# Kernel tuning notes

Hardware: AMD Instinct MI355X
Metric: run time of the kernel (lower is better)

Reference implementation:

```python
import jax, jax.numpy as jnp
import numpy as np

B, S, D, H, F = 2, 2048, 1024, 16, 4096
DH = D // H
EPS = 1e-6


def setup_inputs() -> dict:
    key = jax.random.key(0)
    ks = jax.random.split(key, 8)
    x = jax.random.normal(ks[0], (B, S, D), dtype=jnp.float32)
    # causal mask, broadcastable over [B,H,S,S]
    attention_mask = jnp.tril(jnp.ones((S, S), dtype=bool))[None, None]
    Wqkv = jax.random.normal(ks[1], (3 * D, D), dtype=jnp.float32) * (1.0 / np.sqrt(D))
    Wout = jax.random.normal(ks[2], (D, D), dtype=jnp.float32) * (1.0 / np.sqrt(D))
    W1 = jax.random.normal(ks[3], (F, D), dtype=jnp.float32) * (1.0 / np.sqrt(D))
    b1 = jnp.zeros((F,), dtype=jnp.float32)
    W2 = jax.random.normal(ks[4], (D, F), dtype=jnp.float32) * (1.0 / np.sqrt(F))
    b2 = jnp.zeros((D,), dtype=jnp.float32)
    gamma1 = jnp.ones((D,), dtype=jnp.float32)
    beta1 = jnp.zeros((D,), dtype=jnp.float32)
    gamma2 = jnp.ones((D,), dtype=jnp.float32)
    beta2 = jnp.zeros((D,), dtype=jnp.float32)
    return {"x": x, "attention_mask": attention_mask, "Wqkv": Wqkv, "Wout": Wout,
            "W1": W1, "b1": b1, "W2": W2, "b2": b2,
            "gamma1": gamma1, "beta1": beta1, "gamma2": gamma2, "beta2": beta2}


def layer_norm(x, gamma, beta):
    # Matches torch module: (x - mean) / (std + eps), std unbiased=False
    mean = jnp.mean(x, axis=-1, keepdims=True)
    std = jnp.sqrt(jnp.mean((x - mean) ** 2, axis=-1, keepdims=True))
    return gamma * ((x - mean) / (std + EPS)) + beta


def reference(x, attention_mask, Wqkv, Wout, W1, b1, W2, b2, gamma1, beta1, gamma2, beta2):
    # --- attention sub-block (Pre-LN) ---
    h = layer_norm(x, gamma1, beta1)
    qkv = h @ Wqkv.T                                   # [B,S,3D]
    qkv = qkv.reshape(B, S, 3, H, DH).transpose(2, 0, 3, 1, 4)  # [3,B,H,S,DH]
    q, k, v = qkv[0], qkv[1], qkv[2]
    scale = DH ** -0.5
    scores = jnp.einsum('bhqd,bhkd->bhqk', q, k) * scale
    scores = jnp.where(attention_mask, scores, -jnp.inf)
    attn = jax.nn.softmax(scores, axis=-1)
    out = jnp.einsum('bhqk,bhkd->bhqd', attn, v)       # [B,H,S,DH]
    out = out.transpose(0, 2, 1, 3).reshape(B, S, D)
    out = out @ Wout.T
    x = x + out                                        # dropout eval = identity
    # --- FFN sub-block (Pre-LN) ---
    h = layer_norm(x, gamma2, beta2)
    h = jax.nn.gelu(h @ W1.T + b1, approximate=False)  # torch GELU default = exact erf
    h = h @ W2.T + b2
    return x + h
```

## Files before the change

### kernel.cpp

```cpp
#include <hip/hip_runtime.h>
#include <hip/hip_bf16.h>
#include <math.h>


typedef __bf16 bf16;
typedef __bf16 bf16x4 __attribute__((ext_vector_type(4)));
typedef __bf16 bf16x8 __attribute__((ext_vector_type(8)));
typedef float f32x4 __attribute__((ext_vector_type(4)));

#define LOG2E 1.4426950408889634f
#define NSHIFT -17.312340489f

__device__ __forceinline__ f32x4 mfma16(bf16x8 a, bf16x8 b, f32x4 c) {
    return __builtin_amdgcn_mfma_f32_16x16x32_bf16(a, b, c, 0, 0, 0);
}
__device__ __forceinline__ void load16_lds(const bf16* g, bf16* l) {
    __builtin_amdgcn_global_load_lds(
        (__attribute__((address_space(1))) void*)g,
        (__attribute__((address_space(3))) void*)l, 16, 0, 0);
}

__global__ __launch_bounds__(256) void cvt4_kernel(const float* __restrict__ s0,
                                                   const float* __restrict__ s1,
                                                   const float* __restrict__ s2,
                                                   const float* __restrict__ s3,
                                                   bf16* __restrict__ dst) {
    const int blk = blockIdx.x;
    const float* s;
    int base;
    if (blk < 3072)      { s = s0; base = blk * 1024; }
    else if (blk < 4096) { s = s1; base = (blk - 3072) * 1024; }
    else if (blk < 8192) { s = s2; base = (blk - 4096) * 1024; }
    else                 { s = s3; base = (blk - 8192) * 1024; }
    const int t4 = threadIdx.x * 4;
    const float4 f = *(const float4*)(s + base + t4);
    bf16x4 o;
    o[0] = (bf16)f.x; o[1] = (bf16)f.y; o[2] = (bf16)f.z; o[3] = (bf16)f.w;
    *(bf16x4*)(dst + (size_t)blk * 1024 + t4) = o;
}

__global__ __launch_bounds__(256) void ln_kernel(const float* __restrict__ xin,
                                                 bf16* __restrict__ out,
                                                 const float* __restrict__ gamma,
                                                 const float* __restrict__ beta) {
    const int row = blockIdx.x;
    const int tid = threadIdx.x;
    const float4 f = *(const float4*)(xin + (size_t)row * 1024 + tid * 4);
    float v[4] = {f.x, f.y, f.z, f.w};
    float s = v[0] + v[1] + v[2] + v[3];
    float s2 = v[0] * v[0] + v[1] * v[1] + v[2] * v[2] + v[3] * v[3];
#pragma unroll
    for (int off = 1; off < 64; off <<= 1) {
        s += __shfl_xor(s, off);
        s2 += __shfl_xor(s2, off);
    }
    __shared__ float red[8];
    const int wave = tid >> 6, lane = tid & 63;
    if (lane == 0) { red[wave] = s; red[4 + wave] = s2; }
    __syncthreads();
    s = red[0] + red[1] + red[2] + red[3];
    s2 = red[4] + red[5] + red[6] + red[7];
    const float mean = s * (1.0f / 1024.0f);
    float var = s2 * (1.0f / 1024.0f) - mean * mean;
    var = fmaxf(var, 0.0f);
    const float rstd = 1.0f / (sqrtf(var) + 1e-6f);
    const int c = tid * 4;
    const float4 g = *(const float4*)(gamma + c);
    const float4 b = *(const float4*)(beta + c);
    bf16x4 o;
    o[0] = (bf16)((v[0] - mean) * rstd * g.x + b.x);
    o[1] = (bf16)((v[1] - mean) * rstd * g.y + b.y);
    o[2] = (bf16)((v[2] - mean) * rstd * g.z + b.z);
    o[3] = (bf16)((v[3] - mean) * rstd * g.w + b.w);
    *(bf16x4*)(out + (size_t)row * 1024 + c) = o;
}

#define STAGE(tt, bi)                                              \
    do {                                                           \
        const int _k0 = (tt) << 5;                                 \
        load16_lds(Ap + _k0, &As[bi][tid * 8]);                    \
        load16_lds(Bp + _k0, &Bs[bi][tid * 8]);                    \
        load16_lds(Ap + rstep + _k0, &As[bi][tid * 8 + 2048]);     \
        load16_lds(Bp + rstep + _k0, &Bs[bi][tid * 8 + 2048]);     \
    } while (0)

template <int EPI>
__global__ __launch_bounds__(256, 3) void gemm_bt(const bf16* __restrict__ A,
                                                  const bf16* __restrict__ B,
                                                  int N, int K, int ldk,
                                                  bf16* __restrict__ outb,
                                                  float* __restrict__ outf,
                                                  const float* __restrict__ bias,
                                                  const float* __restrict__ resf,
                                                  bf16* __restrict__ qk,
                                                  bf16* __restrict__ vt) {
    __shared__ alignas(16) bf16 As[3][128 * 32];
    __shared__ alignas(16) bf16 Bs[3][128 * 32];
    const int tid = threadIdx.x;
    const int bm = blockIdx.x, bn = blockIdx.y;
    const int wave = tid >> 6, lane = tid & 63;
    const int wm = (wave >> 1) * 64, wn = (wave & 1) * 64;
    const int l16 = lane & 15, quad = lane >> 4;

    f32x4 acc[4][4] = {};

    const size_t koff = (size_t)blockIdx.z * K;
    const int row0 = tid >> 2, ch0 = tid & 3;
    const int gch = ch0 ^ ((row0 >> 1) & 3);
    const bf16* Ap = A + (size_t)(bm * 128 + row0) * ldk + koff + gch * 8;
    const bf16* Bp = B + (size_t)(bn * 128 + row0) * ldk + koff + gch * 8;
    const size_t rstep = (size_t)64 * ldk;

    const int nt = K >> 5;

    STAGE(0, 0);
    STAGE(1, 1);
    asm volatile("s_waitcnt vmcnt(4)" ::: "memory");
    __builtin_amdgcn_s_barrier();
    asm volatile("" ::: "memory");

    int i0 = 0, i1 = 1, i2 = 2;
    for (int t = 0; t < nt; ++t) {
        if (t + 2 < nt) STAGE(t + 2, i2);

        bf16x8 af[4], bfr[4];
#pragma unroll
        for (int i = 0; i < 4; i++) {
            const int ra = wm + i * 16 + l16;
            af[i] = *(const bf16x8*)(&As[i0][ra * 32 + (quad ^ ((ra >> 1) & 3)) * 8]);
        }
#pragma unroll
        for (int j = 0; j < 4; j++) {
            const int rb = wn + j * 16 + l16;
            bfr[j] = *(const bf16x8*)(&Bs[i0][rb * 32 + (quad ^ ((rb >> 1) & 3)) * 8]);
        }
        __builtin_amdgcn_s_setprio(1);
#pragma unroll
        for (int i = 0; i < 4; i++)
#pragma unroll
            for (int j = 0; j < 4; j++) acc[i][j] = mfma16(af[i], bfr[j], acc[i][j]);
        __builtin_amdgcn_s_setprio(0);

        if (t + 2 < nt) {
            asm volatile("s_waitcnt vmcnt(4)" ::: "memory");
        } else if (t + 1 < nt) {
            asm volatile("s_waitcnt vmcnt(0)" ::: "memory");
        }
        if (t + 1 < nt) {
            __builtin_amdgcn_s_barrier();
            asm volatile("" ::: "memory");
        }
        const int tmp = i0; i0 = i1; i1 = i2; i2 = tmp;
    }

#pragma unroll
    for (int i = 0; i < 4; i++) {
#pragma unroll
        for (int j = 0; j < 4; j++) {
            const int gr0 = bm * 128 + wm + i * 16 + quad * 4;
            const int gc = bn * 128 + wn + j * 16 + l16;
            float bv = 0.0f;
            if (EPI == 2) bv = bias[gc];
            if (EPI == 5 && bias && blockIdx.z == 0) bv = bias[gc];
            if (EPI == 4 && gc >= 2048) {
                const int n = gc - 2048;
                const int hh = n >> 6, dd = n & 63;
                const int bb = gr0 >> 11, ss = gr0 & 2047;
                bf16x4 pk;
#pragma unroll
                for (int r = 0; r < 4; r++) pk[r] = (bf16)acc[i][j][r];
                *(bf16x4*)(vt + ((size_t)((bb * 16 + hh) * 64 + dd)) * 2048 + ss) = pk;
            } else {
#pragma unroll
                for (int r = 0; r < 4; r++) {
                    const float v = acc[i][j][r];
                    const size_t idx = (size_t)(gr0 + r) * N + gc;
                    if (EPI == 0) {
                        outb[idx] = (bf16)v;
                    } else if (EPI == 1) {
                        outf[idx] = v + resf[idx];
                    } else if (EPI == 2) {
                        const float t = v + bv;
                        outb[idx] = (bf16)(0.5f * t * (1.0f + erff(t * 0.70710678118654752f)));
                    } else if (EPI == 5) {
                        atomicAdd(&outf[idx], v + bv);
                    } else {
                        qk[(size_t)(gr0 + r) * 2048 + gc] = (bf16)v;
                    }
                }
            }
        }
    }
}
#undef STAGE

__global__ __launch_bounds__(256, 4) void flash_attn(const bf16* __restrict__ qk,
                                                     const bf16* __restrict__ vt,
                                                     bf16* __restrict__ attn) {
    __shared__ alignas(16) bf16 Ks[64 * 72];
    __shared__ alignas(16) bf16 Vs[64 * 72];
    __shared__ alignas(16) bf16 Ps[4][16 * 72];
    const int tid = threadIdx.x;
    const int wave = tid >> 6, lane = tid & 63;
    const int l16 = lane & 15, quad = lane >> 4;
    const int bh = blockIdx.x;
    const int qt = 31 - blockIdx.y;
    const int b = bh >> 4, h = bh & 15;
    const int q0w = qt * 64 + wave * 16;
    const bf16* qkb = qk + (size_t)b * 2048 * 2048;
    const bf16* vtb = vt + (size_t)bh * 64 * 2048;

    bf16x8 qf[2];
#pragma unroll
    for (int c = 0; c < 2; c++) {
        bf16x8 v = *(const bf16x8*)(qkb + (size_t)(q0w + l16) * 2048 +
                                    h * 64 + c * 32 + quad * 8);
#pragma unroll
        for (int e = 0; e < 8; e++) v[e] = (bf16)((float)v[e] * 0.125f);
        qf[c] = v;
    }

    float lsum[4] = {0.0f, 0.0f, 0.0f, 0.0f};
    f32x4 o[4] = {};

    const int ntiles = qt + 1;
    for (int t = 0; t < ntiles; t++) {
        const int k0 = t * 64;
#pragma unroll
        for (int i = 0; i < 2; i++) {
            const int r = i * 32 + (tid >> 3), ch = tid & 7;
            *(uint4*)(&Ks[r * 72 + ch * 8]) =
                *(const uint4*)(qkb + (size_t)(k0 + r) * 2048 + 1024 + h * 64 + ch * 8);
            *(uint4*)(&Vs[r * 72 + ch * 8]) =
                *(const uint4*)(vtb + (size_t)r * 2048 + k0 + ch * 8);
        }
        __syncthreads();
        f32x4 s[4];
#pragma unroll
        for (int kt = 0; kt < 4; kt++) {
            const bf16x8 k0f = *(const bf16x8*)(&Ks[(kt * 16 + l16) * 72 + quad * 8]);
            const bf16x8 k1f = *(const bf16x8*)(&Ks[(kt * 16 + l16) * 72 + 32 + quad * 8]);
            s[kt] = mfma16(qf[1], k1f, mfma16(qf[0], k0f, (f32x4){0, 0, 0, 0}));
        }
        const bool need_mask = (t == ntiles - 1);
#pragma unroll
        for (int r = 0; r < 4; r++) {
            const int qrow = q0w + quad * 4 + r;
            float e0 = exp2f(fmaf(s[0][r], LOG2E, NSHIFT));
            float e1 = exp2f(fmaf(s[1][r], LOG2E, NSHIFT));
            float e2 = exp2f(fmaf(s[2][r], LOG2E, NSHIFT));
            float e3 = exp2f(fmaf(s[3][r], LOG2E, NSHIFT));
            if (need_mask) {
                if (k0 + l16 > qrow) e0 = 0.0f;
                if (k0 + 16 + l16 > qrow) e1 = 0.0f;
                if (k0 + 32 + l16 > qrow) e2 = 0.0f;
                if (k0 + 48 + l16 > qrow) e3 = 0.0f;
            }
            lsum[r] += (e0 + e1) + (e2 + e3);
            bf16* pp = &Ps[wave][(quad * 4 + r) * 72];
            pp[l16] = (bf16)e0;
            pp[16 + l16] = (bf16)e1;
            pp[32 + l16] = (bf16)e2;
            pp[48 + l16] = (bf16)e3;
        }
#pragma unroll
        for (int c = 0; c < 2; c++) {
            const bf16x8 pf = *(const bf16x8*)(&Ps[wave][l16 * 72 + c * 32 + quad * 8]);
#pragma unroll
            for (int dt = 0; dt < 4; dt++) {
                const bf16x8 vf =
                    *(const bf16x8*)(&Vs[(dt * 16 + l16) * 72 + c * 32 + quad * 8]);
                o[dt] = mfma16(pf, vf, o[dt]);
            }
        }
        __syncthreads();
    }

#pragma unroll
    for (int r = 0; r < 4; r++) {
#pragma unroll
        for (int off = 1; off < 16; off <<= 1) lsum[r] += __shfl_xor(lsum[r], off);
        lsum[r] = 1.0f / fmaxf(lsum[r], 1e-30f);
    }
    bf16* ob = attn + (size_t)b * 2048 * 1024;
#pragma unroll
    for (int dt = 0; dt < 4; dt++)
#pragma unroll
        for (int r = 0; r < 4; r++) {
            const int q = q0w + quad * 4 + r;
            ob[(size_t)q * 1024 + h * 64 + dt * 16 + l16] = (bf16)(o[dt][r] * lsum[r]);
        }
}

extern "C" void kernel_launch(void* const* d_in, const int* in_sizes, int n_in,
                              void* d_out, int out_size, void* d_ws, size_t ws_size,
                              hipStream_t stream) {
    const float* x    = (const float*)d_in[0];
    const float* Wqkv = (const float*)d_in[2];
    const float* Wout = (const float*)d_in[3];
    const float* W1   = (const float*)d_in[4];
    const float* b1   = (const float*)d_in[5];
    const float* W2   = (const float*)d_in[6];
    const float* b2   = (const float*)d_in[7];
    const float* g1   = (const float*)d_in[8];
    const float* be1  = (const float*)d_in[9];
    const float* g2   = (const float*)d_in[10];
    const float* be2  = (const float*)d_in[11];

    char* ws = (char*)d_ws;
    bf16* Wb     = (bf16*)(ws);
    bf16* Wqkv_b = (bf16*)(ws);
    bf16* Wout_b = (bf16*)(ws + (6u << 20));
    bf16* W1_b   = (bf16*)(ws + (8u << 20));
    bf16* W2_b   = (bf16*)(ws + (16u << 20));
    bf16* h      = (bf16*)(ws + (24u << 20));
    bf16* qkbuf  = (bf16*)(ws + (32u << 20));
    bf16* vtbuf  = (bf16*)(ws + (48u << 20));
    bf16* attn   = (bf16*)(ws + (56u << 20));
    bf16* act    = (bf16*)(ws + (32u << 20));
    float* x2    = (float*)d_out;

    cvt4_kernel<<<12288, 256, 0, stream>>>(Wqkv, Wout, W1, W2, Wb);

    ln_kernel<<<4096, 256, 0, stream>>>(x, h, g1, be1);
    gemm_bt<4><<<dim3(32, 24), 256, 0, stream>>>(h, Wqkv_b, 3072, 1024, 1024,
                                                 nullptr, nullptr, nullptr, nullptr,
                                                 qkbuf, vtbuf);
    flash_attn<<<dim3(32, 32), 256, 0, stream>>>(qkbuf, vtbuf, attn);
    gemm_bt<1><<<dim3(32, 8), 256, 0, stream>>>(attn, Wout_b, 1024, 1024, 1024,
                                                nullptr, x2, nullptr, x, nullptr, nullptr);
    ln_kernel<<<4096, 256, 0, stream>>>(x2, h, g2, be2);
    gemm_bt<2><<<dim3(32, 32), 256, 0, stream>>>(h, W1_b, 4096, 1024, 1024,
                                                 act, nullptr, b1, nullptr, nullptr, nullptr);
    gemm_bt<5><<<dim3(32, 8, 2), 256, 0, stream>>>(act, W2_b, 1024, 2048, 4096,
                                                   nullptr, x2, b2, nullptr, nullptr, nullptr);
}
```

Baseline: 392.6 us.

## Add 256x256 eight-wave multi-phase GEMM for QKV and FFN projections

Adds a new GEMM kernel with 256x256 block tiles, 512 threads (8 waves), BK=64 split into two 32-wide halves, double-buffered LDS, and global-to-LDS loads interleaved between four barrier-delimited MFMA phases. It is used for the QKV, FFN1 and FFN2 GEMMs. The W2 GEMM moves from split-K 2 to split-K 4 with atomic accumulation, and the old kernel is kept only for the residual output projection. Larger tiles improve operand reuse and the phased schedule overlaps memory traffic with MFMA. In exchange, grids get much smaller (e.g. 192 or 256 blocks), which can leave CUs idle, and there are more barriers and more atomics.

```diff
diff --git a/kernel.cpp b/kernel.cpp
--- a/kernel.cpp
+++ b/kernel.cpp
@@ -84,16 +84,11 @@
         load16_lds(Bp + rstep + _k0, &Bs[bi][tid * 8 + 2048]);     \
     } while (0)
 
-template <int EPI>
-__global__ __launch_bounds__(256, 3) void gemm_bt(const bf16* __restrict__ A,
-                                                  const bf16* __restrict__ B,
-                                                  int N, int K, int ldk,
-                                                  bf16* __restrict__ outb,
-                                                  float* __restrict__ outf,
-                                                  const float* __restrict__ bias,
-                                                  const float* __restrict__ resf,
-                                                  bf16* __restrict__ qk,
-                                                  bf16* __restrict__ vt) {
+__global__ __launch_bounds__(256, 3) void gemm_res(const bf16* __restrict__ A,
+                                                   const bf16* __restrict__ B,
+                                                   int N, int K, int ldk,
+                                                   float* __restrict__ outf,
+                                                   const float* __restrict__ resf) {
     __shared__ alignas(16) bf16 As[3][128 * 32];
     __shared__ alignas(16) bf16 Bs[3][128 * 32];
     const int tid = threadIdx.x;
@@ -104,11 +99,10 @@
 
     f32x4 acc[4][4] = {};
 
-    const size_t koff = (size_t)blockIdx.z * K;
     const int row0 = tid >> 2, ch0 = tid & 3;
     const int gch = ch0 ^ ((row0 >> 1) & 3);
-    const bf16* Ap = A + (size_t)(bm * 128 + row0) * ldk + koff + gch * 8;
-    const bf16* Bp = B + (size_t)(bn * 128 + row0) * ldk + koff + gch * 8;
+    const bf16* Ap = A + (size_t)(bm * 128 + row0) * ldk + gch * 8;
+    const bf16* Bp = B + (size_t)(bn * 128 + row0) * ldk + gch * 8;
     const size_t rstep = (size_t)64 * ldk;
 
     const int nt = K >> 5;
@@ -154,11 +148,163 @@
     }
 
 #pragma unroll
-    for (int i = 0; i < 4; i++) {
+    for (int i = 0; i < 4; i++)
 #pragma unroll
         for (int j = 0; j < 4; j++) {
             const int gr0 = bm * 128 + wm + i * 16 + quad * 4;
             const int gc = bn * 128 + wn + j * 16 + l16;
+#pragma unroll
+            for (int r = 0; r < 4; r++) {
+                const size_t idx = (size_t)(gr0 + r) * N + gc;
+                outf[idx] = acc[i][j][r] + resf[idx];
+            }
+        }
+}
+#undef STAGE
+
+#define STG_A(bb, rk, tt)                                          \
+    do {                                                           \
+        const int _ko = ((tt) << 6) + ((rk) << 5);                 \
+        load16_lds(Ap + _ko, &As[bb][rk][tid * 8]);                \
+        load16_lds(Ap + rstep + _ko, &As[bb][rk][4096 + tid * 8]); \
+    } while (0)
+#define STG_B(bb, rk, tt)                                          \
+    do {                                                           \
+        const int _ko = ((tt) << 6) + ((rk) << 5);                 \
+        load16_lds(Bp + _ko, &Bs[bb][rk][tid * 8]);                \
+        load16_lds(Bp + rstep + _ko, &Bs[bb][rk][4096 + tid * 8]); \
+    } while (0)
+#define PHASE_OPEN()                       \
+    __builtin_amdgcn_s_barrier();          \
+    asm volatile("" ::: "memory");         \
+    __builtin_amdgcn_s_setprio(1)
+#define PHASE_CLOSE()                      \
+    __builtin_amdgcn_s_setprio(0);         \
+    __builtin_amdgcn_s_barrier();          \
+    asm volatile("" ::: "memory")
+
+template <int EPI>
+__global__ __launch_bounds__(512, 2) void gemm256_8ph(const bf16* __restrict__ A,
+                                                      const bf16* __restrict__ B,
+                                                      int N, int K, int ldk,
+                                                      bf16* __restrict__ outb,
+                                                      float* __restrict__ outf,
+                                                      const float* __restrict__ bias,
+                                                      bf16* __restrict__ qk,
+                                                      bf16* __restrict__ vt) {
+    __shared__ alignas(16) bf16 As[2][2][8192];
+    __shared__ alignas(16) bf16 Bs[2][2][8192];
+    const int tid = threadIdx.x;
+    const int bm = blockIdx.x, bn = blockIdx.y;
+    const int wave = tid >> 6, lane = tid & 63;
+    const int wm = (wave >> 2) * 128, wn = (wave & 3) * 64;
+    const int l16 = lane & 15, quad = lane >> 4;
+
+    f32x4 acc[8][4] = {};
+
+    const size_t koff = (size_t)blockIdx.z * K;
+    const int row0 = tid >> 2;
+    const int gch = (tid & 3) ^ (row0 & 3);
+    const bf16* Ap = A + (size_t)(bm * 256 + row0) * ldk + koff + gch * 8;
+    const bf16* Bp = B + (size_t)(bn * 256 + row0) * ldk + koff + gch * 8;
+    const size_t rstep = (size_t)128 * ldk;
+
+    const int NT = K >> 6;
+
+    STG_A(0, 0, 0); STG_B(0, 0, 0); STG_A(0, 1, 0); STG_B(0, 1, 0);
+    STG_A(1, 0, 1); STG_B(1, 0, 1); STG_A(1, 1, 1);
+    asm volatile("s_waitcnt vmcnt(6)" ::: "memory");
+    __builtin_amdgcn_s_barrier();
+    asm volatile("" ::: "memory");
+
+    for (int t = 0; t < NT; ++t) {
+        const int buf = t & 1;
+        bf16x8 af[8], bj0, bj1;
+
+#pragma unroll
+        for (int i = 0; i < 8; i++) {
+            const int ra = wm + i * 16 + l16;
+            af[i] = *(const bf16x8*)&As[buf][0][ra * 32 + (quad ^ (ra & 3)) * 8];
+        }
+        {
+            const int rb0 = wn + l16, rb1 = wn + 16 + l16;
+            bj0 = *(const bf16x8*)&Bs[buf][0][rb0 * 32 + (quad ^ (rb0 & 3)) * 8];
+            bj1 = *(const bf16x8*)&Bs[buf][0][rb1 * 32 + (quad ^ (rb1 & 3)) * 8];
+        }
+        if (t + 1 < NT) STG_B(buf ^ 1, 1, t + 1);
+        PHASE_OPEN();
+#pragma unroll
+        for (int i = 0; i < 8; i++) {
+            acc[i][0] = mfma16(af[i], bj0, acc[i][0]);
+            acc[i][1] = mfma16(af[i], bj1, acc[i][1]);
+        }
+        PHASE_CLOSE();
+
+        {
+            const int rb2 = wn + 32 + l16, rb3 = wn + 48 + l16;
+            bj0 = *(const bf16x8*)&Bs[buf][0][rb2 * 32 + (quad ^ (rb2 & 3)) * 8];
+            bj1 = *(const bf16x8*)&Bs[buf][0][rb3 * 32 + (quad ^ (rb3 & 3)) * 8];
+        }
+        if (t + 2 < NT) STG_A(buf, 0, t + 2);
+        PHASE_OPEN();
+#pragma unroll
+        for (int i = 0; i < 8; i++) {
+            acc[i][2] = mfma16(af[i], bj0, acc[i][2]);
+            acc[i][3] = mfma16(af[i], bj1, acc[i][3]);
+        }
+        PHASE_CLOSE();
+
+#pragma unroll
+        for (int i = 0; i < 8; i++) {
+            const int ra = wm + i * 16 + l16;
+            af[i] = *(const bf16x8*)&As[buf][1][ra * 32 + (quad ^ (ra & 3)) * 8];
+        }
+        {
+            const int rb0 = wn + l16, rb1 = wn + 16 + l16;
+            bj0 = *(const bf16x8*)&Bs[buf][1][rb0 * 32 + (quad ^ (rb0 & 3)) * 8];
+            bj1 = *(const bf16x8*)&Bs[buf][1][rb1 * 32 + (quad ^ (rb1 & 3)) * 8];
+        }
+        if (t + 2 < NT) STG_B(buf, 0, t + 2);
+        PHASE_OPEN();
+#pragma unroll
+        for (int i = 0; i < 8; i++) {
+            acc[i][0] = mfma16(af[i], bj0, acc[i][0]);
+            acc[i][1] = mfma16(af[i], bj1, acc[i][1]);
+        }
+        PHASE_CLOSE();
+
+        {
+            const int rb2 = wn + 32 + l16, rb3 = wn + 48 + l16;
+            bj0 = *(const bf16x8*)&Bs[buf][1][rb2 * 32 + (quad ^ (rb2 & 3)) * 8];
+            bj1 = *(const bf16x8*)&Bs[buf][1][rb3 * 32 + (quad ^ (rb3 & 3)) * 8];
+        }
+        if (t + 2 < NT) STG_A(buf, 1, t + 2);
+        __builtin_amdgcn_s_barrier();
+        asm volatile("" ::: "memory");
+        __builtin_amdgcn_s_setprio(1);
+#pragma unroll
+        for (int i = 0; i < 8; i++) {
+            acc[i][2] = mfma16(af[i], bj0, acc[i][2]);
+            acc[i][3] = mfma16(af[i], bj1, acc[i][3]);
+        }
+        __builtin_amdgcn_s_setprio(0);
+        if (t + 2 < NT) {
+            asm volatile("s_waitcnt vmcnt(6)" ::: "memory");
+        } else if (t + 1 < NT) {
+            asm volatile("s_waitcnt vmcnt(0)" ::: "memory");
+        }
+        if (t + 1 < NT) {
+            __builtin_amdgcn_s_barrier();
+            asm volatile("" ::: "memory");
+        }
+    }
+
+#pragma unroll
+    for (int i = 0; i < 8; i++) {
+#pragma unroll
+        for (int j = 0; j < 4; j++) {
+            const int gr0 = bm * 256 + wm + i * 16 + quad * 4;
+            const int gc = bn * 256 + wn + j * 16 + l16;
             float bv = 0.0f;
             if (EPI == 2) bv = bias[gc];
             if (EPI == 5 && bias && blockIdx.z == 0) bv = bias[gc];
@@ -175,11 +321,7 @@
                 for (int r = 0; r < 4; r++) {
                     const float v = acc[i][j][r];
                     const size_t idx = (size_t)(gr0 + r) * N + gc;
-                    if (EPI == 0) {
-                        outb[idx] = (bf16)v;
-                    } else if (EPI == 1) {
-                        outf[idx] = v + resf[idx];
-                    } else if (EPI == 2) {
+                    if (EPI == 2) {
                         const float t = v + bv;
                         outb[idx] = (bf16)(0.5f * t * (1.0f + erff(t * 0.70710678118654752f)));
                     } else if (EPI == 5) {
@@ -192,7 +334,10 @@
         }
     }
 }
-#undef STAGE
+#undef STG_A
+#undef STG_B
+#undef PHASE_OPEN
+#undef PHASE_CLOSE
 
 __global__ __launch_bounds__(256, 4) void flash_attn(const bf16* __restrict__ qk,
                                                      const bf16* __restrict__ vt,
@@ -323,15 +468,14 @@
     cvt4_kernel<<<12288, 256, 0, stream>>>(Wqkv, Wout, W1, W2, Wb);
 
     ln_kernel<<<4096, 256, 0, stream>>>(x, h, g1, be1);
-    gemm_bt<4><<<dim3(32, 24), 256, 0, stream>>>(h, Wqkv_b, 3072, 1024, 1024,
-                                                 nullptr, nullptr, nullptr, nullptr,
-                                                 qkbuf, vtbuf);
+    gemm256_8ph<4><<<dim3(16, 12), 512, 0, stream>>>(h, Wqkv_b, 3072, 1024, 1024,
+                                                     nullptr, nullptr, nullptr,
+                                                     qkbuf, vtbuf);
     flash_attn<<<dim3(32, 32), 256, 0, stream>>>(qkbuf, vtbuf, attn);
-    gemm_bt<1><<<dim3(32, 8), 256, 0, stream>>>(attn, Wout_b, 1024, 1024, 1024,
-                                                nullptr, x2, nullptr, x, nullptr, nullptr);
+    gemm_res<<<dim3(32, 8), 256, 0, stream>>>(attn, Wout_b, 1024, 1024, 1024, x2, x);
     ln_kernel<<<4096, 256, 0, stream>>>(x2, h, g2, be2);
-    gemm_bt<2><<<dim3(32, 32), 256, 0, stream>>>(h, W1_b, 4096, 1024, 1024,
-                                                 act, nullptr, b1, nullptr, nullptr, nullptr);
-    gemm_bt<5><<<dim3(32, 8, 2), 256, 0, stream>>>(act, W2_b, 1024, 2048, 4096,
-                                                   nullptr, x2, b2, nullptr, nullptr, nullptr);
-}
+    gemm256_8ph<2><<<dim3(16, 16), 512, 0, stream>>>(h, W1_b, 4096, 1024, 1024,
+                                                     act, nullptr, b1, nullptr, nullptr);
+    gemm256_8ph<5><<<dim3(16, 4, 4), 512, 0, stream>>>(act, W2_b, 1024, 1024, 4096,
+                                                       nullptr, x2, b2, nullptr, nullptr);
+}
```

Result: slower. 407.8 us (+3.9%).

## Use double-buffered GEMM for out-proj and FFN2, add setprio around attention MFMAs

Applied to the files above, without the earlier changes.

Adds a simpler double-buffered GEMM kernel (two LDS stages, one barrier per k-step) and routes the out-projection and FFN-down launches to it. The existing triple-buffered kernel is renamed and kept for the QKV and FFN-up GEMMs. The flash attention kernel raises wave priority around its MFMA sections so matrix work is issued ahead of the softmax and LDS traffic from other waves. The aim is less pipeline overhead on the smaller GEMMs and better MFMA issue in attention, at the cost of shallower prefetch on those two GEMMs.

```diff
diff --git a/kernel.cpp b/kernel.cpp
--- a/kernel.cpp
+++ b/kernel.cpp
@@ -75,6 +75,91 @@
     *(bf16x4*)(out + (size_t)row * 1024 + c) = o;
 }
 
+template <int EPI>
+__global__ __launch_bounds__(256, 3) void gemm_bt(const bf16* __restrict__ A,
+                                                  const bf16* __restrict__ B,
+                                                  int N, int K, int ldk,
+                                                  bf16* __restrict__ outb,
+                                                  float* __restrict__ outf,
+                                                  const float* __restrict__ bias,
+                                                  const float* __restrict__ resf,
+                                                  bf16* __restrict__ qk,
+                                                  bf16* __restrict__ vt) {
+    __shared__ alignas(16) bf16 As[2][128 * 32];
+    __shared__ alignas(16) bf16 Bs[2][128 * 32];
+    const int tid = threadIdx.x;
+    const int bm = blockIdx.x, bn = blockIdx.y;
+    const int wave = tid >> 6, lane = tid & 63;
+    const int wm = (wave >> 1) * 64, wn = (wave & 1) * 64;
+    const int l16 = lane & 15, quad = lane >> 4;
+
+    f32x4 acc[4][4] = {};
+
+    const size_t koff = (size_t)blockIdx.z * K;
+    const int row0 = tid >> 2, ch0 = tid & 3;
+    const int gch = ch0 ^ ((row0 >> 1) & 3);
+    const bf16* Ap = A + (size_t)(bm * 128 + row0) * ldk + koff + gch * 8;
+    const bf16* Bp = B + (size_t)(bn * 128 + row0) * ldk + koff + gch * 8;
+    const size_t rstep = (size_t)64 * ldk;
+
+#pragma unroll
+    for (int r = 0; r < 2; r++) {
+        load16_lds(Ap + r * rstep, &As[0][tid * 8 + r * 2048]);
+        load16_lds(Bp + r * rstep, &Bs[0][tid * 8 + r * 2048]);
+    }
+    __syncthreads();
+
+    int buf = 0;
+    for (int k0 = 0; k0 < K; k0 += 32, buf ^= 1) {
+        if (k0 + 32 < K) {
+#pragma unroll
+            for (int r = 0; r < 2; r++) {
+                load16_lds(Ap + r * rstep + k0 + 32, &As[buf ^ 1][tid * 8 + r * 2048]);
+                load16_lds(Bp + r * rstep + k0 + 32, &Bs[buf ^ 1][tid * 8 + r * 2048]);
+            }
+        }
+        bf16x8 af[4], bfr[4];
+#pragma unroll
+        for (int i = 0; i < 4; i++) {
+            const int ra = wm + i * 16 + l16;
+            af[i] = *(const bf16x8*)(&As[buf][ra * 32 + (quad ^ ((ra >> 1) & 3)) * 8]);
+        }
+#pragma unroll
+        for (int j = 0; j < 4; j++) {
+            const int rb = wn + j * 16 + l16;
+            bfr[j] = *(const bf16x8*)(&Bs[buf][rb * 32 + (quad ^ ((rb >> 1) & 3)) * 8]);
+        }
+#pragma unroll
+        for (int i = 0; i < 4; i++)
+#pragma unroll
+            for (int j = 0; j < 4; j++) acc[i][j] = mfma16(af[i], bfr[j], acc[i][j]);
+        __syncthreads();
+    }
+
+#pragma unroll
+    for (int i = 0; i < 4; i++) {
+#pragma unroll
+        for (int j = 0; j < 4; j++) {
+            const int gr0 = bm * 128 + wm + i * 16 + quad * 4;
+            const int gc = bn * 128 + wn + j * 16 + l16;
+            float bv = 0.0f;
+            if (EPI == 5 && bias && blockIdx.z == 0) bv = bias[gc];
+#pragma unroll
+            for (int r = 0; r < 4; r++) {
+                const float v = acc[i][j][r];
+                const size_t idx = (size_t)(gr0 + r) * N + gc;
+                if (EPI == 1) {
+                    outf[idx] = v + resf[idx];
+                } else if (EPI == 5) {
+                    atomicAdd(&outf[idx], v + bv);
+                } else {
+                    outb[idx] = (bf16)v;
+                }
+            }
+        }
+    }
+}
+
 #define STAGE(tt, bi)                                              \
     do {                                                           \
         const int _k0 = (tt) << 5;                                 \
@@ -85,7 +170,7 @@
     } while (0)
 
 template <int EPI>
-__global__ __launch_bounds__(256, 3) void gemm_bt(const bf16* __restrict__ A,
+__global__ __launch_bounds__(256, 3) void gemm_r3(const bf16* __restrict__ A,
                                                   const bf16* __restrict__ B,
                                                   int N, int K, int ldk,
                                                   bf16* __restrict__ outb,
@@ -161,7 +246,6 @@
             const int gc = bn * 128 + wn + j * 16 + l16;
             float bv = 0.0f;
             if (EPI == 2) bv = bias[gc];
-            if (EPI == 5 && bias && blockIdx.z == 0) bv = bias[gc];
             if (EPI == 4 && gc >= 2048) {
                 const int n = gc - 2048;
                 const int hh = n >> 6, dd = n & 63;
@@ -174,16 +258,10 @@
 #pragma unroll
                 for (int r = 0; r < 4; r++) {
                     const float v = acc[i][j][r];
-                    const size_t idx = (size_t)(gr0 + r) * N + gc;
-                    if (EPI == 0) {
-                        outb[idx] = (bf16)v;
-                    } else if (EPI == 1) {
-                        outf[idx] = v + resf[idx];
-                    } else if (EPI == 2) {
+                    if (EPI == 2) {
                         const float t = v + bv;
-                        outb[idx] = (bf16)(0.5f * t * (1.0f + erff(t * 0.70710678118654752f)));
-                    } else if (EPI == 5) {
-                        atomicAdd(&outf[idx], v + bv);
+                        outb[(size_t)(gr0 + r) * N + gc] =
+                            (bf16)(0.5f * t * (1.0f + erff(t * 0.70710678118654752f)));
                     } else {
                         qk[(size_t)(gr0 + r) * 2048 + gc] = (bf16)v;
                     }
@@ -236,12 +314,14 @@
         }
         __syncthreads();
         f32x4 s[4];
+        __builtin_amdgcn_s_setprio(1);
 #pragma unroll
         for (int kt = 0; kt < 4; kt++) {
             const bf16x8 k0f = *(const bf16x8*)(&Ks[(kt * 16 + l16) * 72 + quad * 8]);
             const bf16x8 k1f = *(const bf16x8*)(&Ks[(kt * 16 + l16) * 72 + 32 + quad * 8]);
             s[kt] = mfma16(qf[1], k1f, mfma16(qf[0], k0f, (f32x4){0, 0, 0, 0}));
         }
+        __builtin_amdgcn_s_setprio(0);
         const bool need_mask = (t == ntiles - 1);
 #pragma unroll
         for (int r = 0; r < 4; r++) {
@@ -263,6 +343,7 @@
             pp[32 + l16] = (bf16)e2;
             pp[48 + l16] = (bf16)e3;
         }
+        __builtin_amdgcn_s_setprio(1);
 #pragma unroll
         for (int c = 0; c < 2; c++) {
             const bf16x8 pf = *(const bf16x8*)(&Ps[wave][l16 * 72 + c * 32 + quad * 8]);
@@ -273,6 +354,7 @@
                 o[dt] = mfma16(pf, vf, o[dt]);
             }
         }
+        __builtin_amdgcn_s_setprio(0);
         __syncthreads();
     }
 
@@ -323,14 +405,14 @@
     cvt4_kernel<<<12288, 256, 0, stream>>>(Wqkv, Wout, W1, W2, Wb);
 
     ln_kernel<<<4096, 256, 0, stream>>>(x, h, g1, be1);
-    gemm_bt<4><<<dim3(32, 24), 256, 0, stream>>>(h, Wqkv_b, 3072, 1024, 1024,
+    gemm_r3<4><<<dim3(32, 24), 256, 0, stream>>>(h, Wqkv_b, 3072, 1024, 1024,
                                                  nullptr, nullptr, nullptr, nullptr,
                                                  qkbuf, vtbuf);
     flash_attn<<<dim3(32, 32), 256, 0, stream>>>(qkbuf, vtbuf, attn);
     gemm_bt<1><<<dim3(32, 8), 256, 0, stream>>>(attn, Wout_b, 1024, 1024, 1024,
                                                 nullptr, x2, nullptr, x, nullptr, nullptr);
     ln_kernel<<<4096, 256, 0, stream>>>(x2, h, g2, be2);
-    gemm_bt<2><<<dim3(32, 32), 256, 0, stream>>>(h, W1_b, 4096, 1024, 1024,
+    gemm_r3<2><<<dim3(32, 32), 256, 0, stream>>>(h, W1_b, 4096, 1024, 1024,
                                                  act, nullptr, b1, nullptr, nullptr, nullptr);
     gemm_bt<5><<<dim3(32, 8, 2), 256, 0, stream>>>(act, W2_b, 1024, 2048, 4096,
                                                    nullptr, x2, b2, nullptr, nullptr, nullptr);
```

New measurement: 378.3 us. 1.04x faster.
